# Performance work log

Hardware: AMD Instinct MI355X
Metric: run time of the kernel (lower is better)

Reference implementation:

```python
import jax, jax.numpy as jnp
import numpy as np

B = 65536      # batch size
H = 256        # hidden_size (args['hid_dim'])
MID = 300      # hard-coded encoder bottleneck in CommonFeatureExtractor
THR = 0.6      # similarity_threshold


def _lin(k, fin, fout):
    return jax.random.normal(k, (fin, fout), jnp.float32) / np.sqrt(fin)


def setup_inputs() -> dict:
    key = jax.random.key(0)
    ks = jax.random.split(key, 24)
    inp = {
        'brics': jax.random.normal(ks[0], (B, H), jnp.float32),
        'function_group': jax.random.normal(ks[1], (B, H), jnp.float32),
        'pharmacophore': jax.random.normal(ks[2], (B, H), jnp.float32),
    }
    # three fp encoders: Linear(H,300) -> ReLU -> (Dropout eval) -> Linear(300,H)
    for n, (k1, k2) in zip(['b', 'f', 'p'], [(ks[3], ks[4]), (ks[5], ks[6]), (ks[7], ks[8])]):
        inp['W1_' + n] = _lin(k1, H, MID)
        inp['b1_' + n] = jnp.zeros((MID,), jnp.float32)
        inp['W2_' + n] = _lin(k2, MID, H)
        inp['b2_' + n] = jnp.zeros((H,), jnp.float32)
    inp['Wg'] = _lin(ks[9], 3 * H, 3)        # weight_generator
    inp['bg_v'] = jnp.zeros((3,), jnp.float32)
    inp['We'] = _lin(ks[10], H, H)           # enhancement_layer
    inp['be_v'] = jnp.zeros((H,), jnp.float32)
    inp['Wf'] = _lin(ks[11], 2 * H, H)       # fusion_layer
    inp['bf_v'] = jnp.zeros((H,), jnp.float32)
    return inp


def _fwd(brics, function_group, pharmacophore,
         W1_b, b1_b, W2_b, b2_b, W1_f, b1_f, W2_f, b2_f, W1_p, b1_p, W2_p, b2_p,
         Wg, bg_v, We, be_v, Wf, bf_v):
    def enc(x, W1, b1, W2, b2):
        return jax.nn.relu(x @ W1 + b1) @ W2 + b2  # dropout in eval mode = identity

    eb = enc(brics, W1_b, b1_b, W2_b, b2_b)
    ef = enc(function_group, W1_f, b1_f, W2_f, b2_f)
    ep = enc(pharmacophore, W1_p, b1_p, W2_p, b2_p)

    fps = jnp.stack([eb, ef, ep], axis=1)                              # [B,3,H]
    fpn = fps / jnp.maximum(jnp.linalg.norm(fps, axis=-1, keepdims=True), 1e-12)

    # the 3 unordered pairs (0,1),(0,2),(1,2); the torch sort is irrelevant
    # because the selected pairs are combined by a permutation-invariant
    # softmax-weighted sum.
    ii = jnp.array([0, 0, 1])
    jj = jnp.array([1, 2, 2])
    elem = fpn[:, ii] * fpn[:, jj]                                     # [B,3,H]
    sims = elem.sum(-1)                                                # [B,3] cosine sims
    pmask = sims > THR
    common = 0.5 * (fps[:, ii] + fps[:, jj]) * (elem > THR)            # [B,3,H]

    has = pmask.any(-1)                                                # [B]
    m = jnp.max(jnp.where(pmask, sims, -jnp.inf), axis=-1, keepdims=True)
    m = jnp.where(jnp.isfinite(m), m, 0.0)
    e = jnp.where(pmask, jnp.exp(sims - m), 0.0)                       # masked softmax
    w = e / jnp.maximum(e.sum(-1, keepdims=True), 1e-12)
    sample_common = (common * w[..., None]).sum(1)                     # [B,H]
    common_features = jnp.where(has[:, None], sample_common, fps.mean(1))

    allc = jnp.concatenate([eb, ef, ep], axis=1)                       # [B,3H]
    fw = jax.nn.softmax(allc @ Wg + bg_v, axis=1)                      # [B,3]
    weighted = eb * fw[:, 0:1] + ef * fw[:, 1:2] + ep * fw[:, 2:3]

    enh = jax.nn.sigmoid(common_features @ We + be_v)
    fused = jnp.concatenate([weighted, common_features * enh], axis=1) @ Wf + bf_v
    return fused


def reference(brics, function_group, pharmacophore,
              W1_b, b1_b, W2_b, b2_b, W1_f, b1_f, W2_f, b2_f, W1_p, b1_p, W2_p, b2_p,
              Wg, bg_v, We, be_v, Wf, bf_v):
    return _fwd(brics, function_group, pharmacophore,
                W1_b, b1_b, W2_b, b2_b, W1_f, b1_f, W2_f, b2_f, W1_p, b1_p, W2_p, b2_p,
                Wg, bg_v, We, be_v, Wf, bf_v)
```

## Files before the change

kernel.cpp:

```cpp
#include <hip/hip_runtime.h>

typedef unsigned short u16;
typedef __bf16 bf16x8 __attribute__((ext_vector_type(8)));
typedef float f32x4 __attribute__((ext_vector_type(4)));

__device__ __forceinline__ float b2f(u16 b){ union{unsigned u; float f;} v; v.u=((unsigned)b)<<16; return v.f; }
__device__ __forceinline__ u16 f2b(float f){ unsigned u=__builtin_bit_cast(unsigned,f); return (u16)((u+0x7fffu+((u>>16)&1u))>>16); }
__device__ __forceinline__ float wred(float v){
  #pragma unroll
  for(int off=32; off>0; off>>=1) v += __shfl_xor(v, off, 64);
  return v;
}
__device__ __forceinline__ void stOut(u16* p, float v){ *p = f2b(v); }
__device__ __forceinline__ void stOut(float* p, float v){ *p = v; }

__device__ __forceinline__ void stageA8(u16* dst, const u16* src){
  *(int4*)dst = *(const int4*)src;
}
__device__ __forceinline__ void stageA8(u16* dst, const float* src){
  float4 a = *(const float4*)src;
  float4 b = *(const float4*)(src+4);
  ushort4 o0; o0.x=f2b(a.x); o0.y=f2b(a.y); o0.z=f2b(a.z); o0.w=f2b(a.w);
  ushort4 o1; o1.x=f2b(b.x); o1.y=f2b(b.y); o1.z=f2b(b.z); o1.w=f2b(b.w);
  *(ushort4*)dst = o0;
  *(ushort4*)(dst+4) = o1;
}

template<int MODE, typename OT, typename AT, bool DUAL>
__global__ __launch_bounds__(256) void gemm_k(
    const AT* __restrict__ A, const AT* __restrict__ A2, int lda,
    const u16* __restrict__ Wt, int K,
    const float* __restrict__ bias, int Nreal,
    OT* __restrict__ C, int ldc,
    const u16* __restrict__ mult, int ldm)
{
  const int LP = 72;
  __shared__ __align__(16) u16 As[128*72];
  __shared__ __align__(16) u16 Bs[64*72];
  const int tid = threadIdx.x;
  const size_t m0 = (size_t)blockIdx.x * 128;
  const int n0 = blockIdx.y * 64;
  const int lane = tid & 63, w = tid >> 6;
  const int lr = lane & 15, quad = lane >> 4;
  const int wr = (w >> 1) * 64, wc = (w & 1) * 32;
  const int KH = K >> 1;

  f32x4 acc[4][2];
  #pragma unroll
  for(int i=0;i<4;++i)
    #pragma unroll
    for(int j=0;j<2;++j) acc[i][j] = (f32x4){0.f,0.f,0.f,0.f};

  for(int k0=0; k0<K; k0+=64){
    const AT* Ap = A;
    int kcol = k0;
    if (DUAL && k0 >= KH) { Ap = A2; kcol = k0 - KH; }
    #pragma unroll
    for(int it=0; it<4; ++it){
      int ch = tid + 256*it; int r = ch>>3, s = (ch&7)*8;
      stageA8(&As[r*LP + s], Ap + (m0+r)*(size_t)lda + kcol + s);
    }
    #pragma unroll
    for(int it=0; it<2; ++it){
      int ch = tid + 256*it; int r = ch>>3, s = (ch&7)*8;
      *(int4*)&Bs[r*LP + s] = *(const int4*)&Wt[(size_t)(n0+r)*K + k0 + s];
    }
    __syncthreads();
    #pragma unroll
    for(int kk=0; kk<64; kk+=32){
      bf16x8 af[4], bfr[2];
      #pragma unroll
      for(int i=0;i<4;++i) af[i]  = *(const bf16x8*)&As[(wr + i*16 + lr)*LP + kk + quad*8];
      #pragma unroll
      for(int j=0;j<2;++j) bfr[j] = *(const bf16x8*)&Bs[(wc + j*16 + lr)*LP + kk + quad*8];
      #pragma unroll
      for(int i=0;i<4;++i)
        #pragma unroll
        for(int j=0;j<2;++j)
          acc[i][j] = __builtin_amdgcn_mfma_f32_16x16x32_bf16(af[i], bfr[j], acc[i][j], 0, 0, 0);
    }
    __syncthreads();
  }
  #pragma unroll
  for(int j=0;j<2;++j){
    int col = n0 + wc + j*16 + lr;
    float bv = (col < Nreal) ? bias[col] : 0.f;
    #pragma unroll
    for(int i=0;i<4;++i){
      #pragma unroll
      for(int r=0;r<4;++r){
        size_t row = m0 + wr + i*16 + quad*4 + r;
        size_t ci = row*(size_t)ldc + col;
        float v = acc[i][j][r] + bv;
        if(MODE==1) v = fmaxf(v, 0.f);
        if(MODE==2){ float mv = b2f(mult[row*(size_t)ldm + col]); v = mv / (1.f + __expf(-v)); }
        stOut(&C[ci], v);
      }
    }
  }
}

struct TPar { const float* src; u16* dst; int K, N, Kp, Np; };
struct TArgs { TPar p[8]; };
__global__ __launch_bounds__(256) void transpose_all(TArgs args){
  TPar p = args.p[blockIdx.y];
  int idx = blockIdx.x*256 + threadIdx.x;
  int total = p.Np * p.Kp;
  if (idx >= total) return;
  int n = idx / p.Kp, k = idx - n*p.Kp;
  u16 v = 0;
  if (n < p.N && k < p.K) v = f2b(p.src[(size_t)k*p.N + n]);
  p.dst[idx] = v;
}

__global__ __launch_bounds__(256) void mid_k(
    const u16* eb, const u16* ef, const u16* ep,
    const float* __restrict__ Wg, const float* __restrict__ bg,
    u16* common, u16* weighted)
{
  const int wid = threadIdx.x >> 6, lane = threadIdx.x & 63;
  const size_t row = (size_t)blockIdx.x * 4 + wid;
  const size_t base = row*256 + lane*4;

  ushort4 vb = *(const ushort4*)(eb + base);
  ushort4 vf = *(const ushort4*)(ef + base);
  ushort4 vp = *(const ushort4*)(ep + base);
  float fb[4] = {b2f(vb.x), b2f(vb.y), b2f(vb.z), b2f(vb.w)};
  float ff[4] = {b2f(vf.x), b2f(vf.y), b2f(vf.z), b2f(vf.w)};
  float fp[4] = {b2f(vp.x), b2f(vp.y), b2f(vp.z), b2f(vp.w)};

  float sb=0, sf=0, sp=0, d01=0, d02=0, d12=0, g0=0, g1=0, g2=0;
  #pragma unroll
  for(int j=0;j<4;++j){
    sb += fb[j]*fb[j]; sf += ff[j]*ff[j]; sp += fp[j]*fp[j];
    d01 += fb[j]*ff[j]; d02 += fb[j]*fp[j]; d12 += ff[j]*fp[j];
  }
  #pragma unroll
  for(int seg=0; seg<3; ++seg){
    const float* x = (seg==0) ? fb : (seg==1) ? ff : fp;
    const float* wg = Wg + ((size_t)seg*256 + lane*4)*3;
    float4 w0 = *(const float4*)(wg);
    float4 w1 = *(const float4*)(wg+4);
    float4 w2 = *(const float4*)(wg+8);
    float wv[12] = {w0.x,w0.y,w0.z,w0.w, w1.x,w1.y,w1.z,w1.w, w2.x,w2.y,w2.z,w2.w};
    #pragma unroll
    for(int j=0;j<4;++j){
      g0 += x[j]*wv[j*3+0];
      g1 += x[j]*wv[j*3+1];
      g2 += x[j]*wv[j*3+2];
    }
  }
  sb=wred(sb); sf=wred(sf); sp=wred(sp);
  d01=wred(d01); d02=wred(d02); d12=wred(d12);
  g0=wred(g0); g1=wred(g1); g2=wred(g2);

  float nb = fmaxf(sqrtf(sb), 1e-12f);
  float nf = fmaxf(sqrtf(sf), 1e-12f);
  float np_ = fmaxf(sqrtf(sp), 1e-12f);
  float s01 = d01/(nb*nf), s02 = d02/(nb*np_), s12 = d12/(nf*np_);

  g0 += bg[0]; g1 += bg[1]; g2 += bg[2];
  float gm = fmaxf(g0, fmaxf(g1, g2));
  float e0 = expf(g0-gm), e1 = expf(g1-gm), e2 = expf(g2-gm);
  float es = e0+e1+e2;
  float fw0 = e0/es, fw1 = e1/es, fw2 = e2/es;

  bool p0 = s01 > 0.6f, p1 = s02 > 0.6f, p2 = s12 > 0.6f;
  bool has = p0 || p1 || p2;
  float mm = -__builtin_inff();
  if(p0) mm = fmaxf(mm, s01);
  if(p1) mm = fmaxf(mm, s02);
  if(p2) mm = fmaxf(mm, s12);
  if(!has) mm = 0.f;
  float q0 = p0 ? expf(s01-mm) : 0.f;
  float q1 = p1 ? expf(s02-mm) : 0.f;
  float q2 = p2 ? expf(s12-mm) : 0.f;
  float qs = fmaxf(q0+q1+q2, 1e-12f);
  float w0 = q0/qs, w1 = q1/qs, w2 = q2/qs;

  float inb = 1.f/nb, invf = 1.f/nf, inp = 1.f/np_;
  u16 co[4], wt[4];
  #pragma unroll
  for(int j=0;j<4;++j){
    float a = fb[j], b = ff[j], c = fp[j];
    float na = a*inb, nbv = b*invf, nc = c*inp;
    float c0 = (na*nbv > 0.6f) ? 0.5f*(a+b) : 0.f;
    float c1 = (na*nc  > 0.6f) ? 0.5f*(a+c) : 0.f;
    float c2 = (nbv*nc > 0.6f) ? 0.5f*(b+c) : 0.f;
    float sc = c0*w0 + c1*w1 + c2*w2;
    float cf = has ? sc : (a+b+c)*(1.f/3.f);
    float wv = a*fw0 + b*fw1 + c*fw2;
    co[j] = f2b(cf); wt[j] = f2b(wv);
  }
  ushort4 oc, ow;
  oc.x=co[0]; oc.y=co[1]; oc.z=co[2]; oc.w=co[3];
  ow.x=wt[0]; ow.y=wt[1]; ow.z=wt[2]; ow.w=wt[3];
  *(ushort4*)(common + base) = oc;
  *(ushort4*)(weighted + base) = ow;
}

extern "C" void kernel_launch(void* const* d_in, const int* in_sizes, int n_in,
                              void* d_out, int out_size, void* d_ws, size_t ws_size,
                              hipStream_t stream) {
  const float* brics = (const float*)d_in[0];
  const float* fg    = (const float*)d_in[1];
  const float* ph    = (const float*)d_in[2];
  const float* W1[3] = {(const float*)d_in[3], (const float*)d_in[7], (const float*)d_in[11]};
  const float* b1[3] = {(const float*)d_in[4], (const float*)d_in[8], (const float*)d_in[12]};
  const float* W2[3] = {(const float*)d_in[5], (const float*)d_in[9], (const float*)d_in[13]};
  const float* b2[3] = {(const float*)d_in[6], (const float*)d_in[10], (const float*)d_in[14]};
  const float* Wg = (const float*)d_in[15];
  const float* bg = (const float*)d_in[16];
  const float* We = (const float*)d_in[17];
  const float* be = (const float*)d_in[18];
  const float* Wf = (const float*)d_in[19];
  const float* bf = (const float*)d_in[20];
  float* out = (float*)d_out;

  const int M = in_sizes[0] / 256;

  char* wsp = (char*)d_ws;
  size_t off = 0;
  auto carve = [&](size_t elems)->u16* {
    u16* p = (u16*)(wsp + off);
    off += ((elems*sizeof(u16)) + 255) & ~(size_t)255;
    return p;
  };
  u16* xb0 = carve((size_t)M*256);
  u16* xb1 = carve((size_t)M*256);
  u16* xb2 = carve((size_t)M*256);
  u16* h   = carve((size_t)M*320);
  u16* Wt1[3], *Wt2[3];
  for(int i=0;i<3;++i) Wt1[i] = carve(320*256);
  for(int i=0;i<3;++i) Wt2[i] = carve(256*320);
  u16* WtE = carve(256*256);
  u16* WtF = carve(256*512);
  (void)ws_size; (void)n_in; (void)out_size;

  TArgs ta;
  for(int i=0;i<3;++i){
    ta.p[i]   = {W1[i], Wt1[i], 256, 300, 256, 320};
    ta.p[3+i] = {W2[i], Wt2[i], 300, 256, 320, 256};
  }
  ta.p[6] = {We, WtE, 256, 256, 256, 256};
  ta.p[7] = {Wf, WtF, 512, 256, 512, 256};
  transpose_all<<<dim3(512, 8), 256, 0, stream>>>(ta);

  const float* xin[3] = {brics, fg, ph};
  u16* encp[3] = {xb0, xb1, xb2};
  for(int i=0;i<3;++i){
    gemm_k<1,u16,float,false><<<dim3(M/128, 5), 256, 0, stream>>>(
        xin[i], nullptr, 256, Wt1[i], 256, b1[i], 300, h, 320, nullptr, 0);
    gemm_k<0,u16,u16,false><<<dim3(M/128, 4), 256, 0, stream>>>(
        h, nullptr, 320, Wt2[i], 320, b2[i], 256, encp[i], 256, nullptr, 0);
  }

  mid_k<<<M/4, 256, 0, stream>>>(xb0, xb1, xb2, Wg, bg, xb2, xb0);

  gemm_k<2,u16,u16,false><<<dim3(M/128, 4), 256, 0, stream>>>(
      xb2, nullptr, 256, WtE, 256, be, 256, xb1, 256, xb2, 256);

  gemm_k<0,float,u16,true><<<dim3(M/128, 4), 256, 0, stream>>>(
      xb0, xb1, 256, WtF, 512, bf, 256, out, 256, nullptr, 0);
}
```

Baseline: 533.0 us.

## Use direct global-to-LDS loads with XOR swizzle, fast math, row-wise transpose

The GEMM kernel now stages bf16 A and weight tiles with global_load_lds (direct global-to-LDS DMA) into unpadded tiles. An XOR swizzle replaces the padding to avoid LDS bank conflicts, and it is applied on both the write and read sides. The goal is to skip the register round trip and shrink shared memory. The mid kernel and the sigmoid epilogue switch to hardware rsq/rcp and __expf, which trade a little precision for fewer instructions. The weight transpose kernel is reorganised so each block handles one output row.

```diff
diff --git a/kernel.cpp b/kernel.cpp
--- a/kernel.cpp
+++ b/kernel.cpp
@@ -14,9 +14,12 @@
 __device__ __forceinline__ void stOut(u16* p, float v){ *p = f2b(v); }
 __device__ __forceinline__ void stOut(float* p, float v){ *p = v; }
 
-__device__ __forceinline__ void stageA8(u16* dst, const u16* src){
-  *(int4*)dst = *(const int4*)src;
-}
+__device__ __forceinline__ void gload_lds16(const void* g, void* l){
+  __builtin_amdgcn_global_load_lds(
+      (const __attribute__((address_space(1))) void*)g,
+      (__attribute__((address_space(3))) void*)l, 16, 0, 0);
+}
+
 __device__ __forceinline__ void stageA8(u16* dst, const float* src){
   float4 a = *(const float4*)src;
   float4 b = *(const float4*)(src+4);
@@ -34,15 +37,15 @@
     OT* __restrict__ C, int ldc,
     const u16* __restrict__ mult, int ldm)
 {
-  const int LP = 72;
-  __shared__ __align__(16) u16 As[128*72];
-  __shared__ __align__(16) u16 Bs[64*72];
+  __shared__ __align__(16) u16 As[128*64];
+  __shared__ __align__(16) u16 Bs[64*64];
   const int tid = threadIdx.x;
   const size_t m0 = (size_t)blockIdx.x * 128;
   const int n0 = blockIdx.y * 64;
   const int lane = tid & 63, w = tid >> 6;
   const int lr = lane & 15, quad = lane >> 4;
   const int wr = (w >> 1) * 64, wc = (w & 1) * 32;
+  const int swz = (lr & 7) << 3;
   const int KH = K >> 1;
 
   f32x4 acc[4][2];
@@ -55,24 +58,41 @@
     const AT* Ap = A;
     int kcol = k0;
     if (DUAL && k0 >= KH) { Ap = A2; kcol = k0 - KH; }
-    #pragma unroll
-    for(int it=0; it<4; ++it){
-      int ch = tid + 256*it; int r = ch>>3, s = (ch&7)*8;
-      stageA8(&As[r*LP + s], Ap + (m0+r)*(size_t)lda + kcol + s);
+
+    if constexpr (__is_same(AT, u16)) {
+      #pragma unroll
+      for(int it=0; it<4; ++it){
+        int cbase = it*256 + w*64;
+        int ch = cbase + lane;
+        int r = ch >> 3;
+        int ce = ((ch & 7) * 8) ^ ((r & 7) << 3);
+        gload_lds16(Ap + (m0+r)*(size_t)lda + kcol + ce, &As[cbase*8]);
+      }
+    } else {
+      #pragma unroll
+      for(int it=0; it<4; ++it){
+        int ch = tid + 256*it; int r = ch>>3, s = (ch&7)*8;
+        stageA8(&As[r*64 + (s ^ ((r&7)<<3))], Ap + (m0+r)*(size_t)lda + kcol + s);
+      }
     }
     #pragma unroll
     for(int it=0; it<2; ++it){
-      int ch = tid + 256*it; int r = ch>>3, s = (ch&7)*8;
-      *(int4*)&Bs[r*LP + s] = *(const int4*)&Wt[(size_t)(n0+r)*K + k0 + s];
+      int cbase = it*256 + w*64;
+      int ch = cbase + lane;
+      int r = ch >> 3;
+      int ce = ((ch & 7) * 8) ^ ((r & 7) << 3);
+      gload_lds16(Wt + (size_t)(n0+r)*K + k0 + ce, &Bs[cbase*8]);
     }
     __syncthreads();
     #pragma unroll
     for(int kk=0; kk<64; kk+=32){
       bf16x8 af[4], bfr[2];
       #pragma unroll
-      for(int i=0;i<4;++i) af[i]  = *(const bf16x8*)&As[(wr + i*16 + lr)*LP + kk + quad*8];
-      #pragma unroll
-      for(int j=0;j<2;++j) bfr[j] = *(const bf16x8*)&Bs[(wc + j*16 + lr)*LP + kk + quad*8];
+      for(int i=0;i<4;++i)
+        af[i]  = *(const bf16x8*)&As[(wr + i*16 + lr)*64 + ((kk + quad*8) ^ swz)];
+      #pragma unroll
+      for(int j=0;j<2;++j)
+        bfr[j] = *(const bf16x8*)&Bs[(wc + j*16 + lr)*64 + ((kk + quad*8) ^ swz)];
       #pragma unroll
       for(int i=0;i<4;++i)
         #pragma unroll
@@ -93,7 +113,10 @@
         size_t ci = row*(size_t)ldc + col;
         float v = acc[i][j][r] + bv;
         if(MODE==1) v = fmaxf(v, 0.f);
-        if(MODE==2){ float mv = b2f(mult[row*(size_t)ldm + col]); v = mv / (1.f + __expf(-v)); }
+        if(MODE==2){
+          float mv = b2f(mult[row*(size_t)ldm + col]);
+          v = mv * __builtin_amdgcn_rcpf(1.f + __expf(-v));
+        }
         stOut(&C[ci], v);
       }
     }
@@ -104,13 +127,13 @@
 struct TArgs { TPar p[8]; };
 __global__ __launch_bounds__(256) void transpose_all(TArgs args){
   TPar p = args.p[blockIdx.y];
-  int idx = blockIdx.x*256 + threadIdx.x;
-  int total = p.Np * p.Kp;
-  if (idx >= total) return;
-  int n = idx / p.Kp, k = idx - n*p.Kp;
-  u16 v = 0;
-  if (n < p.N && k < p.K) v = f2b(p.src[(size_t)k*p.N + n]);
-  p.dst[idx] = v;
+  int n = blockIdx.x;
+  if (n >= p.Np) return;
+  for (int k = threadIdx.x; k < p.Kp; k += 256){
+    u16 v = 0;
+    if (n < p.N && k < p.K) v = f2b(p.src[(size_t)k*p.N + n]);
+    p.dst[(size_t)n*p.Kp + k] = v;
+  }
 }
 
 __global__ __launch_bounds__(256) void mid_k(
@@ -154,16 +177,16 @@
   d01=wred(d01); d02=wred(d02); d12=wred(d12);
   g0=wred(g0); g1=wred(g1); g2=wred(g2);
 
-  float nb = fmaxf(sqrtf(sb), 1e-12f);
-  float nf = fmaxf(sqrtf(sf), 1e-12f);
-  float np_ = fmaxf(sqrtf(sp), 1e-12f);
-  float s01 = d01/(nb*nf), s02 = d02/(nb*np_), s12 = d12/(nf*np_);
+  float inb  = __builtin_amdgcn_rsqf(fmaxf(sb, 1e-24f));
+  float invf = __builtin_amdgcn_rsqf(fmaxf(sf, 1e-24f));
+  float inp  = __builtin_amdgcn_rsqf(fmaxf(sp, 1e-24f));
+  float s01 = d01*inb*invf, s02 = d02*inb*inp, s12 = d12*invf*inp;
 
   g0 += bg[0]; g1 += bg[1]; g2 += bg[2];
   float gm = fmaxf(g0, fmaxf(g1, g2));
-  float e0 = expf(g0-gm), e1 = expf(g1-gm), e2 = expf(g2-gm);
-  float es = e0+e1+e2;
-  float fw0 = e0/es, fw1 = e1/es, fw2 = e2/es;
+  float e0 = __expf(g0-gm), e1 = __expf(g1-gm), e2 = __expf(g2-gm);
+  float res = __builtin_amdgcn_rcpf(e0+e1+e2);
+  float fw0 = e0*res, fw1 = e1*res, fw2 = e2*res;
 
   bool p0 = s01 > 0.6f, p1 = s02 > 0.6f, p2 = s12 > 0.6f;
   bool has = p0 || p1 || p2;
@@ -172,13 +195,12 @@
   if(p1) mm = fmaxf(mm, s02);
   if(p2) mm = fmaxf(mm, s12);
   if(!has) mm = 0.f;
-  float q0 = p0 ? expf(s01-mm) : 0.f;
-  float q1 = p1 ? expf(s02-mm) : 0.f;
-  float q2 = p2 ? expf(s12-mm) : 0.f;
-  float qs = fmaxf(q0+q1+q2, 1e-12f);
-  float w0 = q0/qs, w1 = q1/qs, w2 = q2/qs;
-
-  float inb = 1.f/nb, invf = 1.f/nf, inp = 1.f/np_;
+  float q0 = p0 ? __expf(s01-mm) : 0.f;
+  float q1 = p1 ? __expf(s02-mm) : 0.f;
+  float q2 = p2 ? __expf(s12-mm) : 0.f;
+  float rqs = __builtin_amdgcn_rcpf(fmaxf(q0+q1+q2, 1e-12f));
+  float w0 = q0*rqs, w1 = q1*rqs, w2 = q2*rqs;
+
   u16 co[4], wt[4];
   #pragma unroll
   for(int j=0;j<4;++j){
```

Measured after the change: 522.9 us. No clear change (-1.9%).
